# Performance work log

Hardware: AMD Instinct MI355X
Metric: run time of the kernel (lower is better)

The kernel has to match this reference:

```python
import jax, jax.numpy as jnp
import numpy as np

# bitsandbytes NF4 codebook (16 levels, normalized to [-1, 1])
NF4_CODE = jnp.array([
    -1.0, -0.6961928009986877, -0.5250730514526367, -0.39491748809814453,
    -0.28444138169288635, -0.18477343022823334, -0.09105003625154495, 0.0,
    0.07958029955625534, 0.16093020141124725, 0.24611230194568634,
    0.33791524171829224, 0.44070982933044434, 0.5626170039176941,
    0.7229568362236023, 1.0], dtype=jnp.float32)

BLOCK = 64  # bitsandbytes default quantization blocksize
TOK, DIN, DOUT, RANK = 8192, 4096, 4096, 16
LORA_ALPHA = 16
SCALING = LORA_ALPHA / RANK ** 0.5  # rslora


def setup_inputs() -> dict:
    key = jax.random.key(0)
    k1, k2, k3, k4, k5, k6 = jax.random.split(key, 6)
    x = jax.random.normal(k1, (TOK, DIN), dtype=jnp.float32)
    w_codes = jax.random.randint(k2, (DOUT, DIN), 0, 16, dtype=jnp.int32)
    absmax = jax.random.uniform(k3, (DOUT, DIN // BLOCK), dtype=jnp.float32)
    bias = jax.random.normal(k4, (DOUT,), dtype=jnp.float32)
    lora_A = jax.random.normal(k5, (DIN, RANK), dtype=jnp.float32) * (1.0 / DIN ** 0.5)
    lora_B = jax.random.normal(k6, (RANK, DOUT), dtype=jnp.float32) * 0.02
    return {"x": x, "w_codes": w_codes, "absmax": absmax, "bias": bias,
            "lora_A": lora_A, "lora_B": lora_B}


def reference(x, w_codes, absmax, bias, lora_A, lora_B):
    # Dequantize NF4 base weight: codebook lookup * per-block absmax scale
    # W: [DOUT, DIN], absmax broadcast over blocks of 64 along DIN
    W = NF4_CODE[w_codes] * jnp.repeat(absmax, BLOCK, axis=1)
    base_out = x @ W.T + bias                      # [TOK, DOUT]
    lora_out = (x @ lora_A) @ lora_B               # low-rank path [TOK, DOUT]
    return base_out + lora_out * SCALING
```

## Files before the change

kernel.cpp:

```cpp
#include <hip/hip_runtime.h>
#include <hip/hip_bf16.h>
#include <cstdint>
#include <cstddef>

#define TOK   8192
#define DIN   4096
#define DOUT  4096
#define RANK  16
#define KE    4128

#define BM 256
#define BN 256
#define BKT 32
#define NKT (KE / BKT)
#define NBUF 3

typedef __attribute__((ext_vector_type(8))) short bf16x8;
typedef __attribute__((ext_vector_type(4))) float f32x4;
typedef __attribute__((ext_vector_type(8))) unsigned short u16x8;

__device__ __constant__ float NF4_CODE_D[16] = {
    -1.0f, -0.6961928009986877f, -0.5250730514526367f, -0.39491748809814453f,
    -0.28444138169288635f, -0.18477343022823334f, -0.09105003625154495f, 0.0f,
    0.07958029955625534f, 0.16093020141124725f, 0.24611230194568634f,
    0.33791524171829224f, 0.44070982933044434f, 0.5626170039176941f,
    0.7229568362236023f, 1.0f};

__device__ __forceinline__ unsigned short f2bf(float f) {
    union { float f; unsigned u; } v; v.f = f;
    unsigned u = v.u;
    unsigned r = (u + 0x7FFFu + ((u >> 16) & 1u)) >> 16;
    return (unsigned short)r;
}

__device__ __forceinline__ void async_copy16(const void* g, void* l) {
    __builtin_amdgcn_global_load_lds(
        (const __attribute__((address_space(1))) void*)g,
        (__attribute__((address_space(3))) void*)l,
        16, 0, 0);
}

__global__ __launch_bounds__(256) void prep_x(const float* __restrict__ x,
                                              const float* __restrict__ lora_A,
                                              unsigned short* __restrict__ xe) {
    const int tid = threadIdx.x;
    const int l = tid & 63;
    const int w = tid >> 6;
    const int t0 = blockIdx.x * 16 + w * 4;

    float p[4][16];
#pragma unroll
    for (int a = 0; a < 4; ++a)
#pragma unroll
        for (int r = 0; r < 16; ++r) p[a][r] = 0.f;

    for (int it = 0; it < 16; ++it) {
        const int kb = it * 256 + l * 4;
        float4 xv[4];
#pragma unroll
        for (int a = 0; a < 4; ++a)
            xv[a] = *(const float4*)(x + (size_t)(t0 + a) * DIN + kb);
#pragma unroll
        for (int a = 0; a < 4; ++a) {
            ushort4 s;
            s.x = f2bf(xv[a].x); s.y = f2bf(xv[a].y);
            s.z = f2bf(xv[a].z); s.w = f2bf(xv[a].w);
            *(ushort4*)(xe + (size_t)(t0 + a) * KE + kb) = s;
        }
#pragma unroll
        for (int j = 0; j < 4; ++j) {
            const float4* ap = (const float4*)(lora_A + (size_t)(kb + j) * RANK);
            const float4 a0 = ap[0], a1 = ap[1], a2 = ap[2], a3 = ap[3];
            const float av[16] = {a0.x, a0.y, a0.z, a0.w, a1.x, a1.y, a1.z, a1.w,
                                  a2.x, a2.y, a2.z, a2.w, a3.x, a3.y, a3.z, a3.w};
#pragma unroll
            for (int a = 0; a < 4; ++a) {
                const float xs = (j == 0) ? xv[a].x : (j == 1) ? xv[a].y
                                : (j == 2) ? xv[a].z : xv[a].w;
#pragma unroll
                for (int r = 0; r < 16; ++r) p[a][r] += xs * av[r];
            }
        }
    }

#pragma unroll
    for (int a = 0; a < 4; ++a) {
#pragma unroll
        for (int r = 0; r < 16; ++r) {
            float v = p[a][r];
#pragma unroll
            for (int off = 32; off > 0; off >>= 1) v += __shfl_xor(v, off, 64);
            if (l == r)
                xe[(size_t)(t0 + a) * KE + DIN + r] = f2bf(4.0f * v);
        }
        if (l >= 16 && l < 32)
            xe[(size_t)(t0 + a) * KE + DIN + l] =
                (l == 16) ? (unsigned short)0x3F80u : (unsigned short)0u;
    }
}

__global__ __launch_bounds__(256) void dequant_w(const int* __restrict__ codes,
                                                 const float* __restrict__ absmax,
                                                 unsigned short* __restrict__ we) {
    __shared__ float tab[16];
    if (threadIdx.x < 16) tab[threadIdx.x] = NF4_CODE_D[threadIdx.x];
    __syncthreads();
    const size_t tid = (size_t)blockIdx.x * 256 + threadIdx.x;
    const size_t base = tid * 8;
    const int o = (int)(base >> 12);
    const int k = (int)(base & (DIN - 1));
    const float am = absmax[base >> 6];
    const int4 c0 = *(const int4*)(codes + base);
    const int4 c1 = *(const int4*)(codes + base + 4);
    u16x8 ov;
    ov[0] = f2bf(tab[c0.x] * am);
    ov[1] = f2bf(tab[c0.y] * am);
    ov[2] = f2bf(tab[c0.z] * am);
    ov[3] = f2bf(tab[c0.w] * am);
    ov[4] = f2bf(tab[c1.x] * am);
    ov[5] = f2bf(tab[c1.y] * am);
    ov[6] = f2bf(tab[c1.z] * am);
    ov[7] = f2bf(tab[c1.w] * am);
    *(u16x8*)(we + (size_t)o * KE + k) = ov;
}

__global__ __launch_bounds__(256) void fill_wtail(const float* __restrict__ lora_B,
                                                  const float* __restrict__ bias,
                                                  unsigned short* __restrict__ we) {
    const int o = blockIdx.x * 256 + threadIdx.x;
    if (o >= DOUT) return;
    unsigned short* dst = we + (size_t)o * KE + DIN;
#pragma unroll
    for (int r = 0; r < RANK; ++r) dst[r] = f2bf(lora_B[(size_t)r * DOUT + o]);
    dst[16] = f2bf(bias[o]);
#pragma unroll
    for (int r = 17; r < 32; ++r) dst[r] = 0;
}

__global__ __launch_bounds__(512, 2) void gemm_bt(const unsigned short* __restrict__ A,
                                                  const unsigned short* __restrict__ B,
                                                  float* __restrict__ C) {
    __shared__ __attribute__((aligned(1024))) char smem[NBUF * 32768];

    const int tid = threadIdx.x;
    const int l = tid & 63;
    const int w = tid >> 6;
    const int wm = w >> 2;
    const int wn = w & 3;

    const int tm = blockIdx.x >> 4;
    const int tn = blockIdx.x & 15;
    const int rowBase = tm * BM;
    const int colBase = tn * BN;

    int srow[2], scolb[2], loffs[2];
#pragma unroll
    for (int g = 0; g < 2; ++g) {
        const int loff = g * 8192 + tid * 16;
        const int soff = loff ^ (((loff >> 7) & 7) << 4);
        loffs[g] = loff;
        srow[g] = soff >> 6;
        scolb[g] = soff & 63;
    }

    auto stage = [&](int t) {
        char* Ad = smem + (t % NBUF) * 32768;
        char* Bd = Ad + 16384;
        const int k0 = t * BKT;
#pragma unroll
        for (int g = 0; g < 2; ++g)
            async_copy16((const char*)A + ((size_t)(rowBase + srow[g]) * KE + k0) * 2 + scolb[g],
                         Ad + loffs[g]);
#pragma unroll
        for (int g = 0; g < 2; ++g)
            async_copy16((const char*)B + ((size_t)(colBase + srow[g]) * KE + k0) * 2 + scolb[g],
                         Bd + loffs[g]);
    };

    const int lmask = ((l >> 1) & 7) << 4;
    const int aoff = (((wm * 128 + (l & 15)) * 64) + ((l >> 4) * 16)) ^ lmask;
    const int boff = (((wn * 64 + (l & 15)) * 64) + ((l >> 4) * 16)) ^ lmask;

    f32x4 acc[8][4];
#pragma unroll
    for (int m = 0; m < 8; ++m)
#pragma unroll
        for (int n = 0; n < 4; ++n) acc[m][n] = (f32x4){0.f, 0.f, 0.f, 0.f};

    stage(0);
    stage(1);

    for (int t = 0; t < NKT; ++t) {
        if (t < NKT - 1) {
            asm volatile("s_waitcnt vmcnt(4)" ::: "memory");
        } else {
            asm volatile("s_waitcnt vmcnt(0)" ::: "memory");
        }
        __builtin_amdgcn_s_barrier();
        __builtin_amdgcn_sched_barrier(0);

        if (t + 2 < NKT) stage(t + 2);

        const char* At = smem + (t % NBUF) * 32768;
        const char* Bt = At + 16384;

        bf16x8 bfr[4];
#pragma unroll
        for (int n = 0; n < 4; ++n)
            bfr[n] = *(const bf16x8*)(Bt + boff + n * 1024);
#pragma unroll
        for (int m = 0; m < 8; ++m) {
            const bf16x8 af = *(const bf16x8*)(At + aoff + m * 1024);
#pragma unroll
            for (int n = 0; n < 4; ++n)
                acc[m][n] = __builtin_amdgcn_mfma_f32_16x16x32_bf16(
                    af, bfr[n], acc[m][n], 0, 0, 0);
        }
    }

#pragma unroll
    for (int m = 0; m < 8; ++m) {
        const int rowg = rowBase + wm * 128 + m * 16 + (l >> 4) * 4;
#pragma unroll
        for (int n = 0; n < 4; ++n) {
            const int colg = colBase + wn * 64 + n * 16 + (l & 15);
            float* cp = C + (size_t)rowg * DOUT + colg;
#pragma unroll
            for (int r = 0; r < 4; ++r) cp[(size_t)r * DOUT] = acc[m][n][r];
        }
    }
}

extern "C" void kernel_launch(void* const* d_in, const int* in_sizes, int n_in,
                              void* d_out, int out_size, void* d_ws, size_t ws_size,
                              hipStream_t stream) {
    const float* x      = (const float*)d_in[0];
    const int*   codes  = (const int*)d_in[1];
    const float* absmax = (const float*)d_in[2];
    const float* bias   = (const float*)d_in[3];
    const float* lora_A = (const float*)d_in[4];
    const float* lora_B = (const float*)d_in[5];
    float* out = (float*)d_out;

    unsigned short* xe = (unsigned short*)d_ws;
    unsigned short* we = xe + (size_t)TOK * KE;

    prep_x<<<TOK / 16, 256, 0, stream>>>(x, lora_A, xe);
    dequant_w<<<(DOUT * (size_t)DIN / 8) / 256, 256, 0, stream>>>(codes, absmax, we);
    fill_wtail<<<DOUT / 256, 256, 0, stream>>>(lora_B, bias, we);
    gemm_bt<<<(TOK / BM) * (DOUT / BN), 512, 0, stream>>>(xe, we, out);
}
```

Baseline: 375.5 us.

## Restructure GEMM mainloop into ping-pong half-stages with 4-slot LDS and setprio

Pads the extended K to a multiple of 64 and processes two 32-wide K halves per iteration across four LDS slots. Global loads for A and B are split and issued at different points, interleaved with quarter-tile MFMA groups. Those groups are bracketed by explicit lgkmcnt waits, barriers and s_setprio so that memory traffic overlaps compute across waves. This grows LDS use to 128KB per block, which may limit occupancy below the two blocks per CU requested in launch bounds, and adds extra barriers.

New measurement: 370.1 us. No clear change (-1.4%).

```diff
diff --git a/kernel.cpp b/kernel.cpp
--- a/kernel.cpp
+++ b/kernel.cpp
@@ -7,13 +7,11 @@
 #define DIN   4096
 #define DOUT  4096
 #define RANK  16
-#define KE    4128
+#define KE    4160
+#define NKT64 (KE / 64)
 
 #define BM 256
 #define BN 256
-#define BKT 32
-#define NKT (KE / BKT)
-#define NBUF 3
 
 typedef __attribute__((ext_vector_type(8))) short bf16x8;
 typedef __attribute__((ext_vector_type(4))) float f32x4;
@@ -93,7 +91,7 @@
             if (l == r)
                 xe[(size_t)(t0 + a) * KE + DIN + r] = f2bf(4.0f * v);
         }
-        if (l >= 16 && l < 32)
+        if (l >= 16)
             xe[(size_t)(t0 + a) * KE + DIN + l] =
                 (l == 16) ? (unsigned short)0x3F80u : (unsigned short)0u;
     }
@@ -134,13 +132,13 @@
     for (int r = 0; r < RANK; ++r) dst[r] = f2bf(lora_B[(size_t)r * DOUT + o]);
     dst[16] = f2bf(bias[o]);
 #pragma unroll
-    for (int r = 17; r < 32; ++r) dst[r] = 0;
+    for (int r = 17; r < 64; ++r) dst[r] = 0;
 }
 
 __global__ __launch_bounds__(512, 2) void gemm_bt(const unsigned short* __restrict__ A,
                                                   const unsigned short* __restrict__ B,
                                                   float* __restrict__ C) {
-    __shared__ __attribute__((aligned(1024))) char smem[NBUF * 32768];
+    __shared__ __attribute__((aligned(1024))) char smem[4 * 32768];
 
     const int tid = threadIdx.x;
     const int l = tid & 63;
@@ -163,18 +161,21 @@
         scolb[g] = soff & 63;
     }
 
-    auto stage = [&](int t) {
-        char* Ad = smem + (t % NBUF) * 32768;
-        char* Bd = Ad + 16384;
-        const int k0 = t * BKT;
+    auto stageA = [&](int tt, int kh, int slot) {
+        char* dst = smem + slot * 32768;
+        const int k0 = tt * 64 + kh * 32;
 #pragma unroll
         for (int g = 0; g < 2; ++g)
             async_copy16((const char*)A + ((size_t)(rowBase + srow[g]) * KE + k0) * 2 + scolb[g],
-                         Ad + loffs[g]);
+                         dst + loffs[g]);
+    };
+    auto stageB = [&](int tt, int kh, int slot) {
+        char* dst = smem + slot * 32768 + 16384;
+        const int k0 = tt * 64 + kh * 32;
 #pragma unroll
         for (int g = 0; g < 2; ++g)
             async_copy16((const char*)B + ((size_t)(colBase + srow[g]) * KE + k0) * 2 + scolb[g],
-                         Bd + loffs[g]);
+                         dst + loffs[g]);
     };
 
     const int lmask = ((l >> 1) & 7) << 4;
@@ -187,35 +188,94 @@
 #pragma unroll
         for (int n = 0; n < 4; ++n) acc[m][n] = (f32x4){0.f, 0.f, 0.f, 0.f};
 
-    stage(0);
-    stage(1);
-
-    for (int t = 0; t < NKT; ++t) {
-        if (t < NKT - 1) {
+    stageA(0, 0, 0); stageB(0, 0, 0);
+    stageA(0, 1, 1); stageB(0, 1, 1);
+
+    for (int t = 0; t < NKT64; ++t) {
+        const char* S0 = smem + ((2 * t) & 3) * 32768;
+        const char* S1 = smem + ((2 * t + 1) & 3) * 32768;
+        const int d0 = (2 * t + 2) & 3, d1 = (2 * t + 3) & 3;
+        const bool more = (t + 1 < NKT64);
+
+        bf16x8 bf[4], af[4];
+
+        asm volatile("s_waitcnt vmcnt(4)" ::: "memory");
+        __builtin_amdgcn_s_barrier();
+        __builtin_amdgcn_sched_barrier(0);
+        if (more) stageA(t + 1, 0, d0);
+#pragma unroll
+        for (int n = 0; n < 4; ++n)
+            bf[n] = *(const bf16x8*)(S0 + 16384 + boff + n * 1024);
+#pragma unroll
+        for (int m = 0; m < 4; ++m)
+            af[m] = *(const bf16x8*)(S0 + aoff + m * 1024);
+        asm volatile("s_waitcnt lgkmcnt(0)" ::: "memory");
+        __builtin_amdgcn_sched_barrier(0);
+        __builtin_amdgcn_s_setprio(1);
+#pragma unroll
+        for (int m = 0; m < 4; ++m)
+#pragma unroll
+            for (int n = 0; n < 4; ++n)
+                acc[m][n] = __builtin_amdgcn_mfma_f32_16x16x32_bf16(
+                    af[m], bf[n], acc[m][n], 0, 0, 0);
+        __builtin_amdgcn_s_setprio(0);
+        __builtin_amdgcn_s_barrier();
+
+        if (more) stageB(t + 1, 0, d0);
+#pragma unroll
+        for (int m = 0; m < 4; ++m)
+            af[m] = *(const bf16x8*)(S0 + aoff + (4 + m) * 1024);
+        asm volatile("s_waitcnt lgkmcnt(0)" ::: "memory");
+        __builtin_amdgcn_sched_barrier(0);
+        __builtin_amdgcn_s_setprio(1);
+#pragma unroll
+        for (int m = 0; m < 4; ++m)
+#pragma unroll
+            for (int n = 0; n < 4; ++n)
+                acc[4 + m][n] = __builtin_amdgcn_mfma_f32_16x16x32_bf16(
+                    af[m], bf[n], acc[4 + m][n], 0, 0, 0);
+        __builtin_amdgcn_s_setprio(0);
+
+        if (more) {
             asm volatile("s_waitcnt vmcnt(4)" ::: "memory");
         } else {
             asm volatile("s_waitcnt vmcnt(0)" ::: "memory");
         }
         __builtin_amdgcn_s_barrier();
         __builtin_amdgcn_sched_barrier(0);
-
-        if (t + 2 < NKT) stage(t + 2);
-
-        const char* At = smem + (t % NBUF) * 32768;
-        const char* Bt = At + 16384;
-
-        bf16x8 bfr[4];
+        if (more) stageA(t + 1, 1, d1);
 #pragma unroll
         for (int n = 0; n < 4; ++n)
-            bfr[n] = *(const bf16x8*)(Bt + boff + n * 1024);
-#pragma unroll
-        for (int m = 0; m < 8; ++m) {
-            const bf16x8 af = *(const bf16x8*)(At + aoff + m * 1024);
+            bf[n] = *(const bf16x8*)(S1 + 16384 + boff + n * 1024);
+#pragma unroll
+        for (int m = 0; m < 4; ++m)
+            af[m] = *(const bf16x8*)(S1 + aoff + m * 1024);
+        asm volatile("s_waitcnt lgkmcnt(0)" ::: "memory");
+        __builtin_amdgcn_sched_barrier(0);
+        __builtin_amdgcn_s_setprio(1);
+#pragma unroll
+        for (int m = 0; m < 4; ++m)
 #pragma unroll
             for (int n = 0; n < 4; ++n)
                 acc[m][n] = __builtin_amdgcn_mfma_f32_16x16x32_bf16(
-                    af, bfr[n], acc[m][n], 0, 0, 0);
-        }
+                    af[m], bf[n], acc[m][n], 0, 0, 0);
+        __builtin_amdgcn_s_setprio(0);
+        __builtin_amdgcn_s_barrier();
+
+        if (more) stageB(t + 1, 1, d1);
+#pragma unroll
+        for (int m = 0; m < 4; ++m)
+            af[m] = *(const bf16x8*)(S1 + aoff + (4 + m) * 1024);
+        asm volatile("s_waitcnt lgkmcnt(0)" ::: "memory");
+        __builtin_amdgcn_sched_barrier(0);
+        __builtin_amdgcn_s_setprio(1);
+#pragma unroll
+        for (int m = 0; m < 4; ++m)
+#pragma unroll
+            for (int n = 0; n < 4; ++n)
+                acc[4 + m][n] = __builtin_amdgcn_mfma_f32_16x16x32_bf16(
+                    af[m], bf[n], acc[4 + m][n], 0, 0, 0);
+        __builtin_amdgcn_s_setprio(0);
     }
 
 #pragma unroll
```
